# Optimization experiments

Hardware: AMD Instinct MI355X
Metric: run time of the kernel (lower is better)

Reference implementation:

```python
import jax, jax.numpy as jnp
import numpy as np

N = 50000
E = 800000
T = 5            # towers
F = 10           # in_num / F_in per tower (divide_input=False)
F_OUT = 2        # out_channels // towers
G = 64           # number of graphs in the batch
L = 2            # conv layers
BN_EPS = 1e-5
STD_EPS = 1e-5


def setup_inputs() -> dict:
    key = jax.random.key(0)
    ks = jax.random.split(key, 24)
    s = 0.1
    inp = {
        'x': jax.random.normal(ks[0], (N, F), jnp.float32),
        'edge_emb': jax.random.normal(ks[1], (4, F), jnp.float32) * s,
        'mlp1_w1': jax.random.normal(ks[2], (F, 5), jnp.float32) * s,
        'mlp1_b1': jnp.zeros((5,), jnp.float32),
        'mlp1_w2': jax.random.normal(ks[3], (5, F), jnp.float32) * s,
        'mlp1_b2': jnp.zeros((F,), jnp.float32),
        'enc_w': jax.random.normal(ks[4], (L, F, F), jnp.float32) * s,
        'enc_b': jnp.zeros((L, F), jnp.float32),
        'pre_w': jax.random.normal(ks[5], (L, T, 3 * F, F), jnp.float32) * s,
        'pre_b': jnp.zeros((L, T, F), jnp.float32),
        'post_w': jax.random.normal(ks[6], (L, T, 13 * F, F_OUT), jnp.float32) * s,
        'post_b': jnp.zeros((L, T, F_OUT), jnp.float32),
        'lin_w': jax.random.normal(ks[7], (L, F, F), jnp.float32) * s,
        'lin_b': jnp.zeros((L, F), jnp.float32),
        'bn_gamma': jnp.ones((L, F), jnp.float32),
        'bn_beta': jnp.zeros((L, F), jnp.float32),
        'mlp2_w1': jax.random.normal(ks[8], (F, 5), jnp.float32) * s,
        'mlp2_b1': jnp.zeros((5,), jnp.float32),
        'mlp2_w2': jax.random.normal(ks[9], (5, 1), jnp.float32) * s,
        'mlp2_b2': jnp.zeros((1,), jnp.float32),
        'edge_index': jax.random.randint(ks[10], (2, E), 0, N, jnp.int64),
        'edge_attr': jax.random.randint(ks[11], (E,), 0, 4, jnp.int64),
        'batch': jnp.sort(jax.random.randint(ks[12], (N,), 0, G, jnp.int64)),
    }
    return inp


def reference(x, edge_emb, mlp1_w1, mlp1_b1, mlp1_w2, mlp1_b2,
              enc_w, enc_b, pre_w, pre_b, post_w, post_b, lin_w, lin_b,
              bn_gamma, bn_beta, mlp2_w1, mlp2_b1, mlp2_w2, mlp2_b2,
              edge_index, edge_attr, batch):
    src, dst = edge_index[0], edge_index[1]
    # mlp1: 10 -> 5 -> 10
    h = jax.nn.relu(x @ mlp1_w1 + mlp1_b1) @ mlp1_w2 + mlp1_b2  # [N, F]
    ea = edge_emb[edge_attr]  # [E, F] edge embedding lookup

    # in-degree at target nodes, PNA degree statistics
    deg = jax.ops.segment_sum(jnp.ones((src.shape[0],), h.dtype), dst, num_segments=N)
    d = jnp.clip(deg, 1.0)
    avg_log = jnp.mean(jnp.log(deg + 1.0))  # avg_deg['log'] from degree distribution
    log_d = jnp.log(d + 1.0)
    amp = (log_d / avg_log)[:, None, None]
    att = (avg_log / log_d)[:, None, None]
    has_in = (deg > 0)[:, None, None]
    inv_d = (1.0 / d)[:, None, None]

    for l in range(L):
        e = ea @ enc_w[l] + enc_b[l]  # [E, F]
        # message = pre_nn(cat(x_i, x_j, edge_attr)) per tower (x shared across towers)
        msg_in = jnp.concatenate([h[dst], h[src], e], axis=-1)  # [E, 3F]
        m = jnp.einsum('ef,tfo->eto', msg_in, pre_w[l]) + pre_b[l]  # [E, T, F]
        mean = jax.ops.segment_sum(m, dst, num_segments=N) * inv_d
        mean2 = jax.ops.segment_sum(m * m, dst, num_segments=N) * inv_d
        std = jnp.sqrt(jax.nn.relu(mean2 - mean * mean) + STD_EPS)
        mn = jnp.where(has_in, jax.ops.segment_min(m, dst, num_segments=N), 0.0)
        mx = jnp.where(has_in, jax.ops.segment_max(m, dst, num_segments=N), 0.0)
        agg = jnp.concatenate([mean, mn, mx, std], axis=-1)  # [N, T, 4F]
        agg = jnp.concatenate([agg, agg * amp, agg * att], axis=-1)  # [N, T, 12F]
        xt = jnp.broadcast_to(h[:, None, :], (h.shape[0], T, F))
        o = jnp.concatenate([xt, agg], axis=-1)  # [N, T, 13F]
        o = jnp.einsum('ntf,tfo->nto', o, post_w[l]) + post_b[l]  # [N, T, F_OUT]
        o = o.reshape(o.shape[0], T * F_OUT) @ lin_w[l] + lin_b[l]  # [N, F]
        # train-mode BatchNorm over nodes
        mu = jnp.mean(o, axis=0)
        var = jnp.var(o, axis=0)
        o = (o - mu) / jnp.sqrt(var + BN_EPS) * bn_gamma[l] + bn_beta[l]
        h = jax.nn.relu(o)

    g = jax.ops.segment_sum(h, batch, num_segments=G)  # global_add_pool -> [G, F]
    out = jax.nn.relu(g @ mlp2_w1 + mlp2_b1) @ mlp2_w2 + mlp2_b2  # [G, 1]
    return out
```

## Files before the change

kernel.cpp:

```cpp
#include <hip/hip_runtime.h>
#include <math.h>

#define N_NODES 50000
#define N_EDGES 800000
#define G_GRAPHS 64
#define CONV_BLOCKS 2048
#define BSTRIDE 64
#define CPAD 16

#define WAVE_SYNC() asm volatile("s_waitcnt lgkmcnt(0)" ::: "memory")
#define RFL(v) __builtin_amdgcn_readfirstlane(v)

__global__ void k_mlp1(const float* __restrict__ x,
                       const float* __restrict__ w1, const float* __restrict__ b1,
                       const float* __restrict__ w2, const float* __restrict__ b2,
                       float* __restrict__ h,
                       int* __restrict__ cnt,
                       float* __restrict__ bn_part, float* __restrict__ g,
                       float* __restrict__ avg_log,
                       const float* __restrict__ edge_emb,
                       const float* __restrict__ enc_w, const float* __restrict__ enc_b,
                       const float* __restrict__ pre_w, float* __restrict__ encm,
                       float* __restrict__ u) {
  __shared__ float eo[2][4][10];
  __shared__ float sw[500];
  int tid = threadIdx.x;
  int n = blockIdx.x * blockDim.x + tid;
  if (n < 1280) bn_part[n] = 0.f;
  if (n < G_GRAPHS * 10) g[n] = 0.f;
  if (n == 0) avg_log[0] = 0.f;

  bool act = n < N_NODES;
  float hr[10];
  if (act) {
    cnt[n * CPAD] = 0;
    float xv[10];
#pragma unroll
    for (int k = 0; k < 10; k++) xv[k] = x[n * 10 + k];
    float hid[5];
#pragma unroll
    for (int j = 0; j < 5; j++) {
      float a = b1[j];
#pragma unroll
      for (int k = 0; k < 10; k++) a += xv[k] * w1[k * 5 + j];
      hid[j] = fmaxf(a, 0.f);
    }
#pragma unroll
    for (int f = 0; f < 10; f++) {
      float a = b2[f];
#pragma unroll
      for (int j = 0; j < 5; j++) a += hid[j] * w2[j * 10 + f];
      hr[f] = a;
      h[n * 10 + f] = a;
    }
  }
  for (int j = tid; j < 500; j += 256) {
    int t = j / 100, k = (j / 10) % 10, f = j % 10;
    sw[j] = pre_w[(t * 30 + 10 + k) * 10 + f];
  }
  if (blockIdx.x == 0) {
    for (int i = tid; i < 80; i += 256) {
      int l = i / 40; int a = (i / 10) % 4; int k = i % 10;
      float s = enc_b[l * 10 + k];
      for (int j = 0; j < 10; j++) s += edge_emb[a * 10 + j] * enc_w[(l * 10 + j) * 10 + k];
      eo[l][a][k] = s;
    }
  }
  __syncthreads();
  if (blockIdx.x == 0) {
    for (int i = tid; i < 400; i += 256) {
      int l = i / 200; int a = (i / 50) % 4; int t = (i / 10) % 5; int f = i % 10;
      float s = 0.f;
      for (int k = 0; k < 10; k++) s += eo[l][a][k] * pre_w[((l * 5 + t) * 30 + 20 + k) * 10 + f];
      encm[i] = s;
    }
  }
  if (act) {
    float2* up = (float2*)(u + n * 50);
#pragma unroll
    for (int c0 = 0; c0 < 25; c0++) {
      int ca = 2 * c0, cb = 2 * c0 + 1;
      int ta = ca / 10, fa = ca % 10, tb = cb / 10, fb = cb % 10;
      float a = 0.f, b = 0.f;
#pragma unroll
      for (int k = 0; k < 10; k++) {
        a += hr[k] * sw[ta * 100 + fa + k * 10];
        b += hr[k] * sw[tb * 100 + fb + k * 10];
      }
      up[c0] = make_float2(a, b);
    }
  }
}

__global__ void k_scatter(const int* __restrict__ src, const int* __restrict__ dst,
                          const int* __restrict__ attr,
                          int* __restrict__ cnt, int* __restrict__ epk) {
  int e = blockIdx.x * blockDim.x + threadIdx.x;
  if (e >= N_EDGES) return;
  int d = dst[e];
  int s = src[e];
  int a = attr[e];
  int k = atomicAdd(&cnt[d * CPAD], 1);
  if (k < BSTRIDE) epk[d * BSTRIDE + k] = s | (a << 16);
}

__global__ void k_avg(const int* __restrict__ cnt, float* __restrict__ avg_log) {
  __shared__ float ws[4];
  int tid = threadIdx.x;
  float acc = 0.f;
  for (int n = blockIdx.x * 256 + tid; n < N_NODES; n += gridDim.x * 256)
    acc += __logf((float)cnt[n * CPAD] + 1.f);
#pragma unroll
  for (int d = 32; d >= 1; d >>= 1) acc += __shfl_down(acc, d, 64);
  if ((tid & 63) == 0) ws[tid >> 6] = acc;
  __syncthreads();
  if (tid == 0) atomicAdd(avg_log, ws[0] + ws[1] + ws[2] + ws[3]);
}

__global__ __launch_bounds__(256) void k_conv(
    const float* __restrict__ h,
    const float* __restrict__ u,
    const float* __restrict__ pre_w_l,
    const float* __restrict__ pre_b_l,
    const float* __restrict__ post_w_l,
    const float* __restrict__ post_b_l,
    const float* __restrict__ lin_w_l,
    const float* __restrict__ lin_b_l,
    const float* __restrict__ encm_l,
    const int* __restrict__ cnt,
    const int* __restrict__ epk,
    const float* __restrict__ avg_log_p,
    float* __restrict__ o_buf,
    float* __restrict__ bn_part)
{
  __shared__ float sW[1300];
  __shared__ float sLin[100];
  __shared__ float sLb[10];
  __shared__ float sPb[10];
  __shared__ float sP[4][100];
  __shared__ float sO[4][10];
  __shared__ float bnS[10], bnQ[10];

  int tid = threadIdx.x;
  int wid = tid >> 6, lane = tid & 63;
  for (int i = tid; i < 1300; i += 256) sW[i] = post_w_l[i];
  for (int i = tid; i < 100; i += 256) sLin[i] = lin_w_l[i];
  if (tid < 10) {
    sLb[tid] = lin_b_l[tid];
    sPb[tid] = post_b_l[tid];
    bnS[tid] = 0.f; bnQ[tid] = 0.f;
  }
  __syncthreads();

  int f = lane % 10;
  int t = (lane < 50) ? (lane / 10) : 4;
  int c50 = t * 10 + f;
  float wdst[10];
#pragma unroll
  for (int k = 0; k < 10; k++) wdst[k] = pre_w_l[(t * 30 + k) * 10 + f];
  float em0 = encm_l[c50];
  float em1 = encm_l[50 + c50];
  float em2 = encm_l[100 + c50];
  float em3 = encm_l[150 + c50];
  float preb = pre_b_l[c50];
  float avg_log = avg_log_p[0] * (1.f / N_NODES);

  int gw = blockIdx.x * 4 + wid;
  int GW = gridDim.x * 4;
  int nn = (gw < N_NODES) ? ((N_NODES - 1 - gw) / GW + 1) : 0;

  int dgp = 0;
  if (lane < nn) dgp = cnt[(gw + lane * GW) * CPAD];

  float bnSv = 0.f, bnQv = 0.f;

#define PRE(US, AS, IDX) { int sp_ = __builtin_amdgcn_readlane(pk, (IDX) & 63); \
    AS = sp_ >> 16; US = 0.f; \
    if ((IDX) < deg) US = u[(sp_ & 0xFFFF) * 50 + c50]; }
#define PROC(US, AS) { float em_ = (AS & 2) ? ((AS & 1) ? em3 : em2) : ((AS & 1) ? em1 : em0); \
    float m_ = base + em_ + US; \
    sum += m_; sq = fmaf(m_, m_, sq); mnv = fminf(mnv, m_); mxv = fmaxf(mxv, m_); }

  int nxt_pk = 0;
  if (nn > 0) {
    int deg0 = RFL(__builtin_amdgcn_readlane(dgp, 0));
    if (deg0 > BSTRIDE) deg0 = BSTRIDE;
    if (lane < deg0) nxt_pk = epk[gw * BSTRIDE + lane];
  }

  for (int i = 0; i < nn; i++) {
    int n = gw + i * GW;
    int deg = RFL(__builtin_amdgcn_readlane(dgp, i));
    if (deg > BSTRIDE) deg = BSTRIDE;
    int pk = nxt_pk;
    if (i + 1 < nn) {
      int degN = RFL(__builtin_amdgcn_readlane(dgp, i + 1));
      if (degN > BSTRIDE) degN = BSTRIDE;
      int nN = gw + (i + 1) * GW;
      nxt_pk = (lane < degN) ? epk[nN * BSTRIDE + lane] : 0;
    }

    const float* hn = h + n * 10;
    float2 d0 = *(const float2*)hn;
    float2 d1 = *(const float2*)(hn + 2);
    float2 d2 = *(const float2*)(hn + 4);
    float2 d3 = *(const float2*)(hn + 6);
    float2 d4 = *(const float2*)(hn + 8);
    float xf = hn[f];
    float base = preb
      + d0.x * wdst[0] + d0.y * wdst[1] + d1.x * wdst[2] + d1.y * wdst[3]
      + d2.x * wdst[4] + d2.y * wdst[5] + d3.x * wdst[6] + d3.y * wdst[7]
      + d4.x * wdst[8] + d4.y * wdst[9];

    float sum = 0.f, sq = 0.f, mnv = INFINITY, mxv = -INFINITY;
    {
      float u0, u1, u2, u3, u4, u5, u6, u7;
      int a0, a1, a2, a3, a4, a5, a6, a7;
      PRE(u0, a0, 0) PRE(u1, a1, 1) PRE(u2, a2, 2) PRE(u3, a3, 3)
      PRE(u4, a4, 4) PRE(u5, a5, 5) PRE(u6, a6, 6) PRE(u7, a7, 7)
      int full = deg & ~7;
      int jb = 0;
      for (; jb < full; jb += 8) {
        PROC(u0, a0) PRE(u0, a0, jb + 8)
        PROC(u1, a1) PRE(u1, a1, jb + 9)
        PROC(u2, a2) PRE(u2, a2, jb + 10)
        PROC(u3, a3) PRE(u3, a3, jb + 11)
        PROC(u4, a4) PRE(u4, a4, jb + 12)
        PROC(u5, a5) PRE(u5, a5, jb + 13)
        PROC(u6, a6) PRE(u6, a6, jb + 14)
        PROC(u7, a7) PRE(u7, a7, jb + 15)
      }
      if (jb + 0 < deg) PROC(u0, a0)
      if (jb + 1 < deg) PROC(u1, a1)
      if (jb + 2 < deg) PROC(u2, a2)
      if (jb + 3 < deg) PROC(u3, a3)
      if (jb + 4 < deg) PROC(u4, a4)
      if (jb + 5 < deg) PROC(u5, a5)
      if (jb + 6 < deg) PROC(u6, a6)
    }

    float degf = (float)deg;
    float d = fmaxf(degf, 1.f);
    float inv = 1.f / d;
    float mean = sum * inv;
    float var = sq * inv - mean * mean;
    float stdv = sqrtf(fmaxf(var, 0.f) + 1e-5f);
    if (deg == 0) { mnv = 0.f; mxv = 0.f; }
    float log_d = logf(d + 1.f);
    float amp = log_d / avg_log;
    float att = avg_log / log_d;

    float vv[13];
    vv[0] = xf;
    vv[1] = mean;       vv[2] = mnv;        vv[3] = mxv;        vv[4] = stdv;
    vv[5] = mean * amp; vv[6] = mnv * amp;  vv[7] = mxv * amp;  vv[8] = stdv * amp;
    vv[9] = mean * att; vv[10] = mnv * att; vv[11] = mxv * att; vv[12] = stdv * att;
    float p0 = 0.f, p1 = 0.f;
#pragma unroll
    for (int j = 0; j < 13; j++) {
      const float2 w = *(const float2*)&sW[t * 260 + (f + 10 * j) * 2];
      p0 += vv[j] * w.x; p1 += vv[j] * w.y;
    }
    if (lane < 50) *(float2*)&sP[wid][c50 * 2] = make_float2(p0, p1);
    WAVE_SYNC();
    if (lane < 10) {
      int tt = lane >> 1, c = lane & 1;
      float o = sPb[lane];
#pragma unroll
      for (int ff = 0; ff < 10; ff++) o += sP[wid][(tt * 10 + ff) * 2 + c];
      sO[wid][lane] = o;
    }
    WAVE_SYNC();
    if (lane < 10) {
      float r = sLb[lane];
#pragma unroll
      for (int j = 0; j < 10; j++) r += sO[wid][j] * sLin[j * 10 + lane];
      o_buf[n * 10 + lane] = r;
      bnSv += r; bnQv += r * r;
    }
    WAVE_SYNC();
  }
#undef PRE
#undef PROC

  if (lane < 10) {
    atomicAdd(&bnS[lane], bnSv);
    atomicAdd(&bnQ[lane], bnQv);
  }
  __syncthreads();
  if (tid < 20) {
    float v = (tid < 10) ? bnS[tid] : bnQ[tid - 10];
    atomicAdd(&bn_part[(blockIdx.x & 31) * 20 + tid], v);
  }
}

__global__ __launch_bounds__(256) void k_bnpool(
    const float* __restrict__ o_buf,
    const float* __restrict__ bn_part,
    const float* __restrict__ gamma, const float* __restrict__ beta,
    float* __restrict__ h,
    const int* __restrict__ batch, float* __restrict__ g,
    const float* __restrict__ pre_w_next, float* __restrict__ u,
    int do_u, int do_pool) {
  __shared__ float sS[20];
  __shared__ float sMu[10], sInv[10];
  __shared__ float pool[8][10];
  __shared__ float hrow[25][10];
  __shared__ float sw[500];
  __shared__ int g0s;
  int tid = threadIdx.x;
  int n0 = blockIdx.x * 25;
  if (do_u) {
    for (int j = tid; j < 500; j += 256) {
      int t = j / 100, k = (j / 10) % 10, f = j % 10;
      sw[j] = pre_w_next[(t * 30 + 10 + k) * 10 + f];
    }
  }
  if (tid < 20) {
    float s = 0.f;
    for (int j = 0; j < 32; j++) s += bn_part[j * 20 + tid];
    sS[tid] = s;
  }
  if (tid < 80) pool[tid / 10][tid % 10] = 0.f;
  if (tid == 0) g0s = batch[n0];
  __syncthreads();
  if (tid < 10) {
    float mu = sS[tid] * (1.f / N_NODES);
    float var = sS[10 + tid] * (1.f / N_NODES) - mu * mu;
    sMu[tid] = mu;
    sInv[tid] = 1.f / sqrtf(fmaxf(var, 0.f) + 1e-5f);
  }
  __syncthreads();
  if (tid < 250) {
    int dn = tid / 10, f = tid % 10;
    int n = n0 + dn;
    int i = n * 10 + f;
    float o = (o_buf[i] - sMu[f]) * sInv[f] * gamma[f] + beta[f];
    float r = fmaxf(o, 0.f);
    h[i] = r;
    hrow[dn][f] = r;
    if (do_pool) {
      int dg = batch[n] - g0s;
      if (dg < 8) atomicAdd(&pool[dg][f], r);
      else atomicAdd(&g[(g0s + dg) * 10 + f], r);
    }
  }
  __syncthreads();
  if (do_u && tid < 250) {
#pragma unroll
    for (int it = 0; it < 5; it++) {
      int j = tid + it * 250;
      int node = j / 50, c = j % 50;
      int t = c / 10, f2 = c % 10;
      float acc = 0.f;
#pragma unroll
      for (int k = 0; k < 10; k++) acc += hrow[node][k] * sw[t * 100 + f2 + k * 10];
      u[n0 * 50 + j] = acc;
    }
  }
  if (do_pool) {
    __syncthreads();
    if (tid < 80) {
      float v = pool[tid / 10][tid % 10];
      if (v != 0.f) atomicAdd(&g[(g0s + tid / 10) * 10 + tid % 10], v);
    }
  }
}

__global__ void k_mlp2(const float* __restrict__ g,
                       const float* __restrict__ w1, const float* __restrict__ b1,
                       const float* __restrict__ w2, const float* __restrict__ b2,
                       float* __restrict__ out) {
  int b = threadIdx.x;
  if (b >= G_GRAPHS) return;
  float gv[10];
#pragma unroll
  for (int k = 0; k < 10; k++) gv[k] = g[b * 10 + k];
  float acc = b2[0];
#pragma unroll
  for (int j = 0; j < 5; j++) {
    float a = b1[j];
#pragma unroll
    for (int k = 0; k < 10; k++) a += gv[k] * w1[k * 5 + j];
    acc += fmaxf(a, 0.f) * w2[j];
  }
  out[b] = acc;
}

extern "C" void kernel_launch(void* const* d_in, const int* in_sizes, int n_in,
                              void* d_out, int out_size, void* d_ws, size_t ws_size,
                              hipStream_t stream) {
  const float* x        = (const float*)d_in[0];
  const float* edge_emb = (const float*)d_in[1];
  const float* m1w1 = (const float*)d_in[2];
  const float* m1b1 = (const float*)d_in[3];
  const float* m1w2 = (const float*)d_in[4];
  const float* m1b2 = (const float*)d_in[5];
  const float* enc_w = (const float*)d_in[6];
  const float* enc_b = (const float*)d_in[7];
  const float* pre_w = (const float*)d_in[8];
  const float* pre_b = (const float*)d_in[9];
  const float* post_w = (const float*)d_in[10];
  const float* post_b = (const float*)d_in[11];
  const float* lin_w = (const float*)d_in[12];
  const float* lin_b = (const float*)d_in[13];
  const float* bn_g = (const float*)d_in[14];
  const float* bn_b = (const float*)d_in[15];
  const float* m2w1 = (const float*)d_in[16];
  const float* m2b1 = (const float*)d_in[17];
  const float* m2w2 = (const float*)d_in[18];
  const float* m2b2 = (const float*)d_in[19];
  const int* edge_index = (const int*)d_in[20];
  const int* edge_attr  = (const int*)d_in[21];
  const int* batch      = (const int*)d_in[22];
  const int* src  = edge_index;
  const int* dstp = edge_index + N_EDGES;

  char* ws = (char*)d_ws;
  size_t off = 0;
  auto alloc = [&](size_t bytes) {
    void* p = ws + off;
    off += (bytes + 255) & ~(size_t)255;
    return p;
  };
  float*     h       = (float*)alloc(N_NODES * 10 * sizeof(float));
  float*     o_buf   = (float*)alloc(N_NODES * 10 * sizeof(float));
  float*     u       = (float*)alloc((size_t)(N_NODES * 50 + 64) * sizeof(float));
  int*       cnt     = (int*)alloc((size_t)N_NODES * CPAD * sizeof(int));
  int*       epk     = (int*)alloc((size_t)N_NODES * BSTRIDE * sizeof(int));
  float*     encm    = (float*)alloc(400 * sizeof(float));
  float*     avg_log = (float*)alloc(16);
  float*     bn_part = (float*)alloc(2 * 32 * 20 * sizeof(float));
  float*     g       = (float*)alloc(G_GRAPHS * 10 * sizeof(float));

  k_mlp1<<<(N_NODES + 255) / 256, 256, 0, stream>>>(x, m1w1, m1b1, m1w2, m1b2, h,
                                                    cnt, bn_part, g, avg_log,
                                                    edge_emb, enc_w, enc_b, pre_w, encm, u);
  k_scatter<<<(N_EDGES + 255) / 256, 256, 0, stream>>>(src, dstp, edge_attr, cnt, epk);
  k_avg<<<64, 256, 0, stream>>>(cnt, avg_log);

  for (int l = 0; l < 2; l++) {
    k_conv<<<CONV_BLOCKS, 256, 0, stream>>>(
        h, u, pre_w + l * 1500, pre_b + l * 50, post_w + l * 1300, post_b + l * 10,
        lin_w + l * 100, lin_b + l * 10, encm + l * 200,
        cnt, epk, avg_log, o_buf, bn_part + l * 640);
    k_bnpool<<<N_NODES / 25, 256, 0, stream>>>(
        o_buf, bn_part + l * 640, bn_g + l * 10, bn_b + l * 10, h, batch, g,
        pre_w + 1500, u, l == 0, l == 1);
  }
  k_mlp2<<<1, 64, 0, stream>>>(g, m2w1, m2b1, m2w2, m2b2, (float*)d_out);
}
```

Baseline: 287.6 us.

## Pre-scale edge packing, prefetch next node features, vectorize scatter

```diff
diff --git a/kernel.cpp b/kernel.cpp
--- a/kernel.cpp
+++ b/kernel.cpp
@@ -7,6 +7,7 @@
 #define CONV_BLOCKS 2048
 #define BSTRIDE 64
 #define CPAD 16
+#define ZPACK (N_NODES * 200)
 
 #define WAVE_SYNC() asm volatile("s_waitcnt lgkmcnt(0)" ::: "memory")
 #define RFL(v) __builtin_amdgcn_readfirstlane(v)
@@ -29,6 +30,10 @@
   if (n < 1280) bn_part[n] = 0.f;
   if (n < G_GRAPHS * 10) g[n] = 0.f;
   if (n == 0) avg_log[0] = 0.f;
+  {
+    int z = n - N_NODES;
+    if (z >= 0 && z < 50) u[N_NODES * 50 + z] = 0.f;
+  }
 
   bool act = n < N_NODES;
   float hr[10];
@@ -95,13 +100,19 @@
 __global__ void k_scatter(const int* __restrict__ src, const int* __restrict__ dst,
                           const int* __restrict__ attr,
                           int* __restrict__ cnt, int* __restrict__ epk) {
-  int e = blockIdx.x * blockDim.x + threadIdx.x;
-  if (e >= N_EDGES) return;
-  int d = dst[e];
-  int s = src[e];
-  int a = attr[e];
-  int k = atomicAdd(&cnt[d * CPAD], 1);
-  if (k < BSTRIDE) epk[d * BSTRIDE + k] = s | (a << 16);
+  int e4 = (blockIdx.x * 256 + threadIdx.x) * 4;
+  if (e4 >= N_EDGES) return;
+  const int4 s4 = *(const int4*)(src + e4);
+  const int4 d4 = *(const int4*)(dst + e4);
+  const int4 a4 = *(const int4*)(attr + e4);
+  int k0 = atomicAdd(&cnt[d4.x * CPAD], 1);
+  int k1 = atomicAdd(&cnt[d4.y * CPAD], 1);
+  int k2 = atomicAdd(&cnt[d4.z * CPAD], 1);
+  int k3 = atomicAdd(&cnt[d4.w * CPAD], 1);
+  if (k0 < BSTRIDE) epk[d4.x * BSTRIDE + k0] = s4.x * 200 + a4.x;
+  if (k1 < BSTRIDE) epk[d4.y * BSTRIDE + k1] = s4.y * 200 + a4.y;
+  if (k2 < BSTRIDE) epk[d4.z * BSTRIDE + k2] = s4.z * 200 + a4.z;
+  if (k3 < BSTRIDE) epk[d4.w * BSTRIDE + k3] = s4.w * 200 + a4.w;
 }
 
 __global__ void k_avg(const int* __restrict__ cnt, float* __restrict__ avg_log) {
@@ -117,7 +128,7 @@
   if (tid == 0) atomicAdd(avg_log, ws[0] + ws[1] + ws[2] + ws[3]);
 }
 
-__global__ __launch_bounds__(256) void k_conv(
+__global__ __launch_bounds__(256, 8) void k_conv(
     const float* __restrict__ h,
     const float* __restrict__ u,
     const float* __restrict__ pre_w_l,
@@ -155,6 +166,7 @@
   int f = lane % 10;
   int t = (lane < 50) ? (lane / 10) : 4;
   int c50 = t * 10 + f;
+  const char* ub = (const char*)u;
   float wdst[10];
 #pragma unroll
   for (int k = 0; k < 10; k++) wdst[k] = pre_w_l[(t * 30 + k) * 10 + f];
@@ -175,17 +187,26 @@
   float bnSv = 0.f, bnQv = 0.f;
 
 #define PRE(US, AS, IDX) { int sp_ = __builtin_amdgcn_readlane(pk, (IDX) & 63); \
-    AS = sp_ >> 16; US = 0.f; \
-    if ((IDX) < deg) US = u[(sp_ & 0xFFFF) * 50 + c50]; }
-#define PROC(US, AS) { float em_ = (AS & 2) ? ((AS & 1) ? em3 : em2) : ((AS & 1) ? em1 : em0); \
-    float m_ = base + em_ + US; \
+    AS = sp_ & 3; \
+    const float* row_ = (const float*)(ub + (sp_ & ~7)); \
+    US = row_[c50]; }
+#define PROC(US, AS) { float m_ = ((AS & 2) ? ((AS & 1) ? bem3 : bem2) : ((AS & 1) ? bem1 : bem0)) + US; \
     sum += m_; sq = fmaf(m_, m_, sq); mnv = fminf(mnv, m_); mxv = fmaxf(mxv, m_); }
 
-  int nxt_pk = 0;
+  int nxt_pk = ZPACK;
+  float2 ph0, ph1, ph2, ph3, ph4;
+  float pxf = 0.f;
   if (nn > 0) {
     int deg0 = RFL(__builtin_amdgcn_readlane(dgp, 0));
     if (deg0 > BSTRIDE) deg0 = BSTRIDE;
-    if (lane < deg0) nxt_pk = epk[gw * BSTRIDE + lane];
+    nxt_pk = (lane < deg0) ? epk[gw * BSTRIDE + lane] : ZPACK;
+    const float* hn = h + gw * 10;
+    ph0 = *(const float2*)hn;
+    ph1 = *(const float2*)(hn + 2);
+    ph2 = *(const float2*)(hn + 4);
+    ph3 = *(const float2*)(hn + 6);
+    ph4 = *(const float2*)(hn + 8);
+    pxf = hn[f];
   }
 
   for (int i = 0; i < nn; i++) {
@@ -193,24 +214,27 @@
     int deg = RFL(__builtin_amdgcn_readlane(dgp, i));
     if (deg > BSTRIDE) deg = BSTRIDE;
     int pk = nxt_pk;
+    float2 d0 = ph0, d1 = ph1, d2 = ph2, d3 = ph3, d4 = ph4;
+    float xf = pxf;
     if (i + 1 < nn) {
       int degN = RFL(__builtin_amdgcn_readlane(dgp, i + 1));
       if (degN > BSTRIDE) degN = BSTRIDE;
-      int nN = gw + (i + 1) * GW;
-      nxt_pk = (lane < degN) ? epk[nN * BSTRIDE + lane] : 0;
-    }
-
-    const float* hn = h + n * 10;
-    float2 d0 = *(const float2*)hn;
-    float2 d1 = *(const float2*)(hn + 2);
-    float2 d2 = *(const float2*)(hn + 4);
-    float2 d3 = *(const float2*)(hn + 6);
-    float2 d4 = *(const float2*)(hn + 8);
-    float xf = hn[f];
+      int nN = n + GW;
+      nxt_pk = (lane < degN) ? epk[nN * BSTRIDE + lane] : ZPACK;
+      const float* hn2 = h + nN * 10;
+      ph0 = *(const float2*)hn2;
+      ph1 = *(const float2*)(hn2 + 2);
+      ph2 = *(const float2*)(hn2 + 4);
+      ph3 = *(const float2*)(hn2 + 6);
+      ph4 = *(const float2*)(hn2 + 8);
+      pxf = hn2[f];
+    }
+
     float base = preb
       + d0.x * wdst[0] + d0.y * wdst[1] + d1.x * wdst[2] + d1.y * wdst[3]
       + d2.x * wdst[4] + d2.y * wdst[5] + d3.x * wdst[6] + d3.y * wdst[7]
       + d4.x * wdst[8] + d4.y * wdst[9];
+    float bem0 = base + em0, bem1 = base + em1, bem2 = base + em2, bem3 = base + em3;
 
     float sum = 0.f, sq = 0.f, mnv = INFINITY, mxv = -INFINITY;
     {
@@ -436,7 +460,7 @@
   k_mlp1<<<(N_NODES + 255) / 256, 256, 0, stream>>>(x, m1w1, m1b1, m1w2, m1b2, h,
                                                     cnt, bn_part, g, avg_log,
                                                     edge_emb, enc_w, enc_b, pre_w, encm, u);
-  k_scatter<<<(N_EDGES + 255) / 256, 256, 0, stream>>>(src, dstp, edge_attr, cnt, epk);
+  k_scatter<<<(N_EDGES / 4 + 255) / 256, 256, 0, stream>>>(src, dstp, edge_attr, cnt, epk);
   k_avg<<<64, 256, 0, stream>>>(cnt, avg_log);
 
   for (int l = 0; l < 2; l++) {
```

New measurement: 311.7 us. +8.4%, slower.

## Assign one node per wave in conv kernel and pre-scale packed edge offsets

Applied to the files above, without the earlier changes.

```diff
diff --git a/kernel.cpp b/kernel.cpp
--- a/kernel.cpp
+++ b/kernel.cpp
@@ -4,7 +4,6 @@
 #define N_NODES 50000
 #define N_EDGES 800000
 #define G_GRAPHS 64
-#define CONV_BLOCKS 2048
 #define BSTRIDE 64
 #define CPAD 16
 
@@ -101,7 +100,7 @@
   int s = src[e];
   int a = attr[e];
   int k = atomicAdd(&cnt[d * CPAD], 1);
-  if (k < BSTRIDE) epk[d * BSTRIDE + k] = s | (a << 16);
+  if (k < BSTRIDE) epk[d * BSTRIDE + k] = s * 200 + a;
 }
 
 __global__ void k_avg(const int* __restrict__ cnt, float* __restrict__ avg_log) {
@@ -142,7 +141,8 @@
   __shared__ float bnS[10], bnQ[10];
 
   int tid = threadIdx.x;
-  int wid = tid >> 6, lane = tid & 63;
+  int wid = RFL(tid >> 6);
+  int lane = tid & 63;
   for (int i = tid; i < 1300; i += 256) sW[i] = post_w_l[i];
   for (int i = tid; i < 100; i += 256) sLin[i] = lin_w_l[i];
   if (tid < 10) {
@@ -155,6 +155,8 @@
   int f = lane % 10;
   int t = (lane < 50) ? (lane / 10) : 4;
   int c50 = t * 10 + f;
+  const char* ub = (const char*)u;
+  int c50_4 = c50 * 4;
   float wdst[10];
 #pragma unroll
   for (int k = 0; k < 10; k++) wdst[k] = pre_w_l[(t * 30 + k) * 10 + f];
@@ -165,40 +167,19 @@
   float preb = pre_b_l[c50];
   float avg_log = avg_log_p[0] * (1.f / N_NODES);
 
-  int gw = blockIdx.x * 4 + wid;
-  int GW = gridDim.x * 4;
-  int nn = (gw < N_NODES) ? ((N_NODES - 1 - gw) / GW + 1) : 0;
-
-  int dgp = 0;
-  if (lane < nn) dgp = cnt[(gw + lane * GW) * CPAD];
-
+  int n = blockIdx.x * 4 + wid;
   float bnSv = 0.f, bnQv = 0.f;
 
 #define PRE(US, AS, IDX) { int sp_ = __builtin_amdgcn_readlane(pk, (IDX) & 63); \
-    AS = sp_ >> 16; US = 0.f; \
-    if ((IDX) < deg) US = u[(sp_ & 0xFFFF) * 50 + c50]; }
-#define PROC(US, AS) { float em_ = (AS & 2) ? ((AS & 1) ? em3 : em2) : ((AS & 1) ? em1 : em0); \
-    float m_ = base + em_ + US; \
+    AS = sp_ & 3; US = 0.f; \
+    if ((IDX) < deg) US = *(const float*)(ub + (sp_ & ~7) + c50_4); }
+#define PROC(US, AS) { float m_ = ((AS & 2) ? ((AS & 1) ? bem3 : bem2) : ((AS & 1) ? bem1 : bem0)) + US; \
     sum += m_; sq = fmaf(m_, m_, sq); mnv = fminf(mnv, m_); mxv = fmaxf(mxv, m_); }
 
-  int nxt_pk = 0;
-  if (nn > 0) {
-    int deg0 = RFL(__builtin_amdgcn_readlane(dgp, 0));
-    if (deg0 > BSTRIDE) deg0 = BSTRIDE;
-    if (lane < deg0) nxt_pk = epk[gw * BSTRIDE + lane];
-  }
-
-  for (int i = 0; i < nn; i++) {
-    int n = gw + i * GW;
-    int deg = RFL(__builtin_amdgcn_readlane(dgp, i));
+  if (n < N_NODES) {
+    int deg = cnt[n * CPAD];
     if (deg > BSTRIDE) deg = BSTRIDE;
-    int pk = nxt_pk;
-    if (i + 1 < nn) {
-      int degN = RFL(__builtin_amdgcn_readlane(dgp, i + 1));
-      if (degN > BSTRIDE) degN = BSTRIDE;
-      int nN = gw + (i + 1) * GW;
-      nxt_pk = (lane < degN) ? epk[nN * BSTRIDE + lane] : 0;
-    }
+    int pk = (lane < deg) ? epk[n * BSTRIDE + lane] : 0;
 
     const float* hn = h + n * 10;
     float2 d0 = *(const float2*)hn;
@@ -207,10 +188,12 @@
     float2 d3 = *(const float2*)(hn + 6);
     float2 d4 = *(const float2*)(hn + 8);
     float xf = hn[f];
+
     float base = preb
       + d0.x * wdst[0] + d0.y * wdst[1] + d1.x * wdst[2] + d1.y * wdst[3]
       + d2.x * wdst[4] + d2.y * wdst[5] + d3.x * wdst[6] + d3.y * wdst[7]
       + d4.x * wdst[8] + d4.y * wdst[9];
+    float bem0 = base + em0, bem1 = base + em1, bem2 = base + em2, bem3 = base + em3;
 
     float sum = 0.f, sq = 0.f, mnv = INFINITY, mxv = -INFINITY;
     {
@@ -276,9 +259,8 @@
 #pragma unroll
       for (int j = 0; j < 10; j++) r += sO[wid][j] * sLin[j * 10 + lane];
       o_buf[n * 10 + lane] = r;
-      bnSv += r; bnQv += r * r;
-    }
-    WAVE_SYNC();
+      bnSv = r; bnQv = r * r;
+    }
   }
 #undef PRE
 #undef PROC
@@ -440,7 +422,7 @@
   k_avg<<<64, 256, 0, stream>>>(cnt, avg_log);
 
   for (int l = 0; l < 2; l++) {
-    k_conv<<<CONV_BLOCKS, 256, 0, stream>>>(
+    k_conv<<<(N_NODES + 3) / 4, 256, 0, stream>>>(
         h, u, pre_w + l * 1500, pre_b + l * 50, post_w + l * 1300, post_b + l * 10,
         lin_w + l * 100, lin_b + l * 10, encm + l * 200,
         cnt, epk, avg_log, o_buf, bn_part + l * 640);
```

Measured after the change: 293.1 us. Within noise of the previous version (+1.9%).
